# Kernel optimization log

Hardware: AMD Instinct MI355X
Metric: run time of the kernel (lower is better)

Reference implementation:

```python
import jax, jax.numpy as jnp
import numpy as np

ALPHA = 0.2  # LeakyReLU negative slope
NEG_INF = -9e15

def setup_inputs() -> dict:
    key = jax.random.key(0)
    k1, k2, k3, k4 = jax.random.split(key, 4)
    N, F_in, F_out = 8192, 256, 64
    h = jax.random.normal(k1, (N, F_in), dtype=jnp.float32)
    adj = jax.random.randint(k2, (N, N), 0, 2, dtype=jnp.int32)
    # xavier_uniform with gain=1.414
    def xavier(k, shape, gain=1.414):
        fan_in, fan_out = shape[0], shape[1]
        limit = gain * np.sqrt(6.0 / (fan_in + fan_out))
        return jax.random.uniform(k, shape, jnp.float32, -limit, limit)
    W = xavier(k3, (F_in, F_out))
    a = xavier(k4, (2 * F_out, 1))
    return {"h": h, "adj": adj, "W": W, "a": a}

def reference(h, adj, W, a):
    # Wh: (N, F_out)
    Wh = h @ W
    F_out = Wh.shape[1]
    a1 = a[:F_out, 0]   # (F_out,)
    a2 = a[F_out:, 0]   # (F_out,)
    # e_ij = LeakyReLU(Wh_i . a1 + Wh_j . a2)  -- equivalent to a^T [Wh_i || Wh_j]
    e = jax.nn.leaky_relu((Wh @ a1)[:, None] + (Wh @ a2)[None, :], negative_slope=ALPHA)
    scores = jnp.where(adj > 0, e, NEG_INF)
    attention = jax.nn.softmax(scores, axis=1)  # (N, N)
    h_prime = attention @ Wh                    # (N, F_out)
    return jax.nn.elu(h_prime)  # concat=True path
```

## Files before the change

### kernel.cpp

```cpp
#include <hip/hip_runtime.h>
#include <hip/hip_bf16.h>

#define N 8192
#define FIN 256
#define FOUT 64
#define NSLICE 8
#define SLICE_J (N / NSLICE)
#define NEG_INF -9.0e15f

typedef __attribute__((ext_vector_type(8))) short short8;
typedef __attribute__((ext_vector_type(4))) float f32x4;

static __device__ __forceinline__ short f2bf(float v) {
    __hip_bfloat16 b = __float2bfloat16(v);
    return __builtin_bit_cast(short, b);
}
static __device__ __forceinline__ float bf2f(short s) {
    unsigned u = ((unsigned)(unsigned short)s) << 16;
    return __builtin_bit_cast(float, u);
}

__global__ __launch_bounds__(256) void k_wh(const float* __restrict__ h,
                                            const float* __restrict__ W,
                                            const float* __restrict__ a,
                                            float* __restrict__ Wh,
                                            float* __restrict__ s1,
                                            float* __restrict__ s2) {
    int wave = threadIdx.x >> 6, lane = threadIdx.x & 63;
    int i = blockIdx.x * 4 + wave;
    const float* hrow = h + (size_t)i * FIN;
    float acc = 0.f;
#pragma unroll 8
    for (int k = 0; k < FIN; k += 4) {
        float4 hv = *(const float4*)(hrow + k);
        acc += hv.x * W[(k + 0) * FOUT + lane];
        acc += hv.y * W[(k + 1) * FOUT + lane];
        acc += hv.z * W[(k + 2) * FOUT + lane];
        acc += hv.w * W[(k + 3) * FOUT + lane];
    }
    Wh[(size_t)i * FOUT + lane] = acc;
    float v1 = acc * a[lane];
    float v2 = acc * a[FOUT + lane];
#pragma unroll
    for (int off = 32; off; off >>= 1) {
        v1 += __shfl_xor(v1, off);
        v2 += __shfl_xor(v2, off);
    }
    if (lane == 0) { s1[i] = v1; s2[i] = v2; }
}

__global__ __launch_bounds__(256) void k_repack(const float* __restrict__ Wh,
                                                short* __restrict__ WhB) {
    int t = blockIdx.x * 256 + threadIdx.x;
    int lane = t & 63, ft = (t >> 6) & 3, jt = t >> 8;
    int g = lane >> 4, r = lane & 15;
    short8 w;
#pragma unroll
    for (int q = 0; q < 8; ++q) {
        float v = Wh[(size_t)(jt * 32 + g * 8 + q) * FOUT + ft * 16 + r];
        w[q] = f2bf(v);
    }
    *((short8*)WhB + t) = w;
}

__global__ __launch_bounds__(128) void k_flash(const int* __restrict__ adj,
                                               const short* __restrict__ WhB,
                                               const float* __restrict__ s1,
                                               const float* __restrict__ s2,
                                               float* __restrict__ pO,
                                               float* __restrict__ pm,
                                               float* __restrict__ pl) {
    int rb = blockIdx.x / NSLICE, sl = blockIdx.x % NSLICE;
    int wave = threadIdx.x >> 6, lane = threadIdx.x & 63;
    int r = lane & 15, g = lane >> 4;
    int row = rb * 32 + wave * 16 + r;

    __shared__ __align__(16) float s2s[SLICE_J];
    for (int t = threadIdx.x; t < SLICE_J; t += 128) s2s[t] = s2[sl * SLICE_J + t];
    __syncthreads();

    float s1i = s1[row];
    float m = NEG_INF, l = 0.f;
    f32x4 acc0 = {0.f, 0.f, 0.f, 0.f};
    f32x4 acc1 = {0.f, 0.f, 0.f, 0.f};
    f32x4 acc2 = {0.f, 0.f, 0.f, 0.f};
    f32x4 acc3 = {0.f, 0.f, 0.f, 0.f};

    const int* arow = adj + (size_t)row * N + sl * SLICE_J + g * 8;

    for (int step = 0; step < SLICE_J / 32; ++step) {
        int4 av0 = *(const int4*)(arow + step * 32);
        int4 av1 = *(const int4*)(arow + step * 32 + 4);
        float4 sv0 = *(const float4*)&s2s[step * 32 + g * 8];
        float4 sv1 = *(const float4*)&s2s[step * 32 + g * 8 + 4];

        auto ec = [&](int aval, float s2v) -> float {
            float x = s1i + s2v;
            x = x > 0.f ? x : 0.2f * x;
            return aval > 0 ? x : NEG_INF;
        };
        float e0 = ec(av0.x, sv0.x), e1 = ec(av0.y, sv0.y);
        float e2 = ec(av0.z, sv0.z), e3 = ec(av0.w, sv0.w);
        float e4 = ec(av1.x, sv1.x), e5 = ec(av1.y, sv1.y);
        float e6 = ec(av1.z, sv1.z), e7 = ec(av1.w, sv1.w);

        float cmax = fmaxf(fmaxf(fmaxf(e0, e1), fmaxf(e2, e3)),
                           fmaxf(fmaxf(e4, e5), fmaxf(e6, e7)));
        cmax = fmaxf(cmax, __shfl_xor(cmax, 16));
        cmax = fmaxf(cmax, __shfl_xor(cmax, 32));
        float mnew = fmaxf(m, cmax);
        float scale = __expf(m - mnew);

        short8 af;
        float csum = 0.f;
        {
            float p0 = __expf(e0 - mnew), p1 = __expf(e1 - mnew);
            float p2 = __expf(e2 - mnew), p3 = __expf(e3 - mnew);
            float p4 = __expf(e4 - mnew), p5 = __expf(e5 - mnew);
            float p6 = __expf(e6 - mnew), p7 = __expf(e7 - mnew);
            af[0] = f2bf(p0); af[1] = f2bf(p1); af[2] = f2bf(p2); af[3] = f2bf(p3);
            af[4] = f2bf(p4); af[5] = f2bf(p5); af[6] = f2bf(p6); af[7] = f2bf(p7);
            csum = bf2f(af[0]) + bf2f(af[1]) + bf2f(af[2]) + bf2f(af[3]) +
                   bf2f(af[4]) + bf2f(af[5]) + bf2f(af[6]) + bf2f(af[7]);
        }
        csum += __shfl_xor(csum, 16);
        csum += __shfl_xor(csum, 32);
        l = l * scale + csum;
        m = mnew;

        float sc0 = __shfl(scale, g * 4 + 0);
        float sc1 = __shfl(scale, g * 4 + 1);
        float sc2 = __shfl(scale, g * 4 + 2);
        float sc3 = __shfl(scale, g * 4 + 3);
        acc0[0] *= sc0; acc0[1] *= sc1; acc0[2] *= sc2; acc0[3] *= sc3;
        acc1[0] *= sc0; acc1[1] *= sc1; acc1[2] *= sc2; acc1[3] *= sc3;
        acc2[0] *= sc0; acc2[1] *= sc1; acc2[2] *= sc2; acc2[3] *= sc3;
        acc3[0] *= sc0; acc3[1] *= sc1; acc3[2] *= sc2; acc3[3] *= sc3;

        int jt = sl * (SLICE_J / 32) + step;
        const short8* bp = (const short8*)WhB + (size_t)jt * 256 + lane;
        acc0 = __builtin_amdgcn_mfma_f32_16x16x32_bf16(af, bp[0], acc0, 0, 0, 0);
        acc1 = __builtin_amdgcn_mfma_f32_16x16x32_bf16(af, bp[64], acc1, 0, 0, 0);
        acc2 = __builtin_amdgcn_mfma_f32_16x16x32_bf16(af, bp[128], acc2, 0, 0, 0);
        acc3 = __builtin_amdgcn_mfma_f32_16x16x32_bf16(af, bp[192], acc3, 0, 0, 0);
    }

    int base_row = rb * 32 + wave * 16;
    f32x4 accs[4] = {acc0, acc1, acc2, acc3};
#pragma unroll
    for (int nt = 0; nt < 4; ++nt) {
#pragma unroll
        for (int reg = 0; reg < 4; ++reg) {
            int orow = base_row + g * 4 + reg;
            pO[((size_t)orow * NSLICE + sl) * FOUT + nt * 16 + r] = accs[nt][reg];
        }
    }
    if (lane < 16) {
        pm[(size_t)row * NSLICE + sl] = m;
        pl[(size_t)row * NSLICE + sl] = l;
    }
}

__global__ __launch_bounds__(256) void k_merge(const float* __restrict__ pO,
                                               const float* __restrict__ pm,
                                               const float* __restrict__ pl,
                                               float* __restrict__ out) {
    int t = blockIdx.x * 256 + threadIdx.x;
    int row = t >> 6, f = t & 63;
    float ms[NSLICE];
    float M = NEG_INF;
#pragma unroll
    for (int s = 0; s < NSLICE; ++s) {
        ms[s] = pm[(size_t)row * NSLICE + s];
        M = fmaxf(M, ms[s]);
    }
    float L = 0.f, O = 0.f;
#pragma unroll
    for (int s = 0; s < NSLICE; ++s) {
        float w = __expf(ms[s] - M);
        L += pl[(size_t)row * NSLICE + s] * w;
        O += pO[((size_t)row * NSLICE + s) * FOUT + f] * w;
    }
    float x = O / L;
    out[t] = x > 0.f ? x : expm1f(x);
}

extern "C" void kernel_launch(void* const* d_in, const int* in_sizes, int n_in,
                              void* d_out, int out_size, void* d_ws, size_t ws_size,
                              hipStream_t stream) {
    const float* h   = (const float*)d_in[0];
    const int*   adj = (const int*)d_in[1];
    const float* W   = (const float*)d_in[2];
    const float* a   = (const float*)d_in[3];
    float* out = (float*)d_out;

    char* ws = (char*)d_ws;
    float* Wh  = (float*)ws;
    short* WhB = (short*)(ws + (2u << 20));
    float* s1  = (float*)(ws + (3u << 20));
    float* s2  = (float*)(ws + (3u << 20) + 32768);
    float* pO  = (float*)(ws + (4u << 20));
    float* pm  = (float*)(ws + (20u << 20));
    float* pl  = (float*)(ws + (20u << 20) + (256u << 10));

    k_wh<<<N / 4, 256, 0, stream>>>(h, W, a, Wh, s1, s2);
    k_repack<<<(N / 32) * 4 * 64 / 256, 256, 0, stream>>>(Wh, WhB);
    k_flash<<<(N / 32) * NSLICE, 128, 0, stream>>>(adj, WhB, s1, s2, pO, pm, pl);
    k_merge<<<N * FOUT / 256, 256, 0, stream>>>(pO, pm, pl, out);
}
```

Measured before the change: 122.2 us.

## Replace online softmax with precomputed global row max bound

```diff
diff --git a/kernel.cpp b/kernel.cpp
--- a/kernel.cpp
+++ b/kernel.cpp
@@ -7,6 +7,7 @@
 #define NSLICE 8
 #define SLICE_J (N / NSLICE)
 #define NEG_INF -9.0e15f
+#define L2E 1.4426950408889634f
 
 typedef __attribute__((ext_vector_type(8))) short short8;
 typedef __attribute__((ext_vector_type(4))) float f32x4;
@@ -18,6 +19,9 @@
 static __device__ __forceinline__ float bf2f(short s) {
     unsigned u = ((unsigned)(unsigned short)s) << 16;
     return __builtin_bit_cast(float, u);
+}
+static __device__ __forceinline__ float exp2fast(float x) {
+    return __builtin_amdgcn_exp2f(x);
 }
 
 __global__ __launch_bounds__(256) void k_wh(const float* __restrict__ h,
@@ -46,7 +50,23 @@
         v1 += __shfl_xor(v1, off);
         v2 += __shfl_xor(v2, off);
     }
-    if (lane == 0) { s1[i] = v1; s2[i] = v2; }
+    if (lane == 0) { s1[i] = v1 * L2E; s2[i] = v2 * L2E; }
+}
+
+__global__ __launch_bounds__(256) void k_max(const float* __restrict__ s2,
+                                             float* __restrict__ maxs2) {
+    int t = threadIdx.x;
+    float m = NEG_INF;
+    for (int i = t; i < N; i += 256) m = fmaxf(m, s2[i]);
+#pragma unroll
+    for (int off = 32; off; off >>= 1) m = fmaxf(m, __shfl_xor(m, off));
+    __shared__ float red[4];
+    if ((t & 63) == 0) red[t >> 6] = m;
+    __syncthreads();
+    if (t == 0) {
+        float r = fmaxf(fmaxf(red[0], red[1]), fmaxf(red[2], red[3]));
+        maxs2[0] = r;
+    }
 }
 
 __global__ __launch_bounds__(256) void k_repack(const float* __restrict__ Wh,
@@ -67,8 +87,8 @@
                                                const short* __restrict__ WhB,
                                                const float* __restrict__ s1,
                                                const float* __restrict__ s2,
+                                               const float* __restrict__ maxs2,
                                                float* __restrict__ pO,
-                                               float* __restrict__ pm,
                                                float* __restrict__ pl) {
     int rb = blockIdx.x / NSLICE, sl = blockIdx.x % NSLICE;
     int wave = threadIdx.x >> 6, lane = threadIdx.x & 63;
@@ -80,7 +100,10 @@
     __syncthreads();
 
     float s1i = s1[row];
-    float m = NEG_INF, l = 0.f;
+    float xm = s1i + maxs2[0];
+    float Mp = fmaxf(xm, 0.2f * xm);
+
+    float l = 0.f;
     f32x4 acc0 = {0.f, 0.f, 0.f, 0.f};
     f32x4 acc1 = {0.f, 0.f, 0.f, 0.f};
     f32x4 acc2 = {0.f, 0.f, 0.f, 0.f};
@@ -88,54 +111,28 @@
 
     const int* arow = adj + (size_t)row * N + sl * SLICE_J + g * 8;
 
+#pragma unroll 2
     for (int step = 0; step < SLICE_J / 32; ++step) {
         int4 av0 = *(const int4*)(arow + step * 32);
         int4 av1 = *(const int4*)(arow + step * 32 + 4);
         float4 sv0 = *(const float4*)&s2s[step * 32 + g * 8];
         float4 sv1 = *(const float4*)&s2s[step * 32 + g * 8 + 4];
 
-        auto ec = [&](int aval, float s2v) -> float {
+        short8 af;
+        auto pc = [&](int aval, float s2v) -> short {
             float x = s1i + s2v;
-            x = x > 0.f ? x : 0.2f * x;
-            return aval > 0 ? x : NEG_INF;
+            float lr = fmaxf(x, 0.2f * x);
+            float p = exp2fast(lr - Mp);
+            p = aval > 0 ? p : 0.f;
+            return f2bf(p);
         };
-        float e0 = ec(av0.x, sv0.x), e1 = ec(av0.y, sv0.y);
-        float e2 = ec(av0.z, sv0.z), e3 = ec(av0.w, sv0.w);
-        float e4 = ec(av1.x, sv1.x), e5 = ec(av1.y, sv1.y);
-        float e6 = ec(av1.z, sv1.z), e7 = ec(av1.w, sv1.w);
+        af[0] = pc(av0.x, sv0.x); af[1] = pc(av0.y, sv0.y);
+        af[2] = pc(av0.z, sv0.z); af[3] = pc(av0.w, sv0.w);
+        af[4] = pc(av1.x, sv1.x); af[5] = pc(av1.y, sv1.y);
+        af[6] = pc(av1.z, sv1.z); af[7] = pc(av1.w, sv1.w);
 
-        float cmax = fmaxf(fmaxf(fmaxf(e0, e1), fmaxf(e2, e3)),
-                           fmaxf(fmaxf(e4, e5), fmaxf(e6, e7)));
-        cmax = fmaxf(cmax, __shfl_xor(cmax, 16));
-        cmax = fmaxf(cmax, __shfl_xor(cmax, 32));
-        float mnew = fmaxf(m, cmax);
-        float scale = __expf(m - mnew);
-
-        short8 af;
-        float csum = 0.f;
-        {
-            float p0 = __expf(e0 - mnew), p1 = __expf(e1 - mnew);
-            float p2 = __expf(e2 - mnew), p3 = __expf(e3 - mnew);
-            float p4 = __expf(e4 - mnew), p5 = __expf(e5 - mnew);
-            float p6 = __expf(e6 - mnew), p7 = __expf(e7 - mnew);
-            af[0] = f2bf(p0); af[1] = f2bf(p1); af[2] = f2bf(p2); af[3] = f2bf(p3);
-            af[4] = f2bf(p4); af[5] = f2bf(p5); af[6] = f2bf(p6); af[7] = f2bf(p7);
-            csum = bf2f(af[0]) + bf2f(af[1]) + bf2f(af[2]) + bf2f(af[3]) +
-                   bf2f(af[4]) + bf2f(af[5]) + bf2f(af[6]) + bf2f(af[7]);
-        }
-        csum += __shfl_xor(csum, 16);
-        csum += __shfl_xor(csum, 32);
-        l = l * scale + csum;
-        m = mnew;
-
-        float sc0 = __shfl(scale, g * 4 + 0);
-        float sc1 = __shfl(scale, g * 4 + 1);
-        float sc2 = __shfl(scale, g * 4 + 2);
-        float sc3 = __shfl(scale, g * 4 + 3);
-        acc0[0] *= sc0; acc0[1] *= sc1; acc0[2] *= sc2; acc0[3] *= sc3;
-        acc1[0] *= sc0; acc1[1] *= sc1; acc1[2] *= sc2; acc1[3] *= sc3;
-        acc2[0] *= sc0; acc2[1] *= sc1; acc2[2] *= sc2; acc2[3] *= sc3;
-        acc3[0] *= sc0; acc3[1] *= sc1; acc3[2] *= sc2; acc3[3] *= sc3;
+        l += bf2f(af[0]) + bf2f(af[1]) + bf2f(af[2]) + bf2f(af[3]) +
+             bf2f(af[4]) + bf2f(af[5]) + bf2f(af[6]) + bf2f(af[7]);
 
         int jt = sl * (SLICE_J / 32) + step;
         const short8* bp = (const short8*)WhB + (size_t)jt * 256 + lane;
@@ -144,6 +141,9 @@
         acc2 = __builtin_amdgcn_mfma_f32_16x16x32_bf16(af, bp[128], acc2, 0, 0, 0);
         acc3 = __builtin_amdgcn_mfma_f32_16x16x32_bf16(af, bp[192], acc3, 0, 0, 0);
     }
+
+    l += __shfl_xor(l, 16);
+    l += __shfl_xor(l, 32);
 
     int base_row = rb * 32 + wave * 16;
     f32x4 accs[4] = {acc0, acc1, acc2, acc3};
@@ -155,31 +155,19 @@
             pO[((size_t)orow * NSLICE + sl) * FOUT + nt * 16 + r] = accs[nt][reg];
         }
     }
-    if (lane < 16) {
-        pm[(size_t)row * NSLICE + sl] = m;
-        pl[(size_t)row * NSLICE + sl] = l;
-    }
+    if (lane < 16) pl[(size_t)row * NSLICE + sl] = l;
 }
 
 __global__ __launch_bounds__(256) void k_merge(const float* __restrict__ pO,
-                                               const float* __restrict__ pm,
                                                const float* __restrict__ pl,
                                                float* __restrict__ out) {
     int t = blockIdx.x * 256 + threadIdx.x;
     int row = t >> 6, f = t & 63;
-    float ms[NSLICE];
-    float M = NEG_INF;
-#pragma unroll
-    for (int s = 0; s < NSLICE; ++s) {
-        ms[s] = pm[(size_t)row * NSLICE + s];
-        M = fmaxf(M, ms[s]);
-    }
     float L = 0.f, O = 0.f;
 #pragma unroll
     for (int s = 0; s < NSLICE; ++s) {
-        float w = __expf(ms[s] - M);
-        L += pl[(size_t)row * NSLICE + s] * w;
-        O += pO[((size_t)row * NSLICE + s) * FOUT + f] * w;
+        L += pl[(size_t)row * NSLICE + s];
+        O += pO[((size_t)row * NSLICE + s) * FOUT + f];
     }
     float x = O / L;
     out[t] = x > 0.f ? x : expm1f(x);
@@ -195,16 +183,17 @@
     float* out = (float*)d_out;
 
     char* ws = (char*)d_ws;
-    float* Wh  = (float*)ws;
-    short* WhB = (short*)(ws + (2u << 20));
-    float* s1  = (float*)(ws + (3u << 20));
-    float* s2  = (float*)(ws + (3u << 20) + 32768);
-    float* pO  = (float*)(ws + (4u << 20));
-    float* pm  = (float*)(ws + (20u << 20));
-    float* pl  = (float*)(ws + (20u << 20) + (256u << 10));
+    float* Wh    = (float*)ws;
+    short* WhB   = (short*)(ws + (2u << 20));
+    float* s1    = (float*)(ws + (3u << 20));
+    float* s2    = (float*)(ws + (3u << 20) + 32768);
+    float* maxs2 = (float*)(ws + (3u << 20) + 65536);
+    float* pO    = (float*)(ws + (4u << 20));
+    float* pl    = (float*)(ws + (20u << 20));
 
     k_wh<<<N / 4, 256, 0, stream>>>(h, W, a, Wh, s1, s2);
+    k_max<<<1, 256, 0, stream>>>(s2, maxs2);
     k_repack<<<(N / 32) * 4 * 64 / 256, 256, 0, stream>>>(Wh, WhB);
-    k_flash<<<(N / 32) * NSLICE, 128, 0, stream>>>(adj, WhB, s1, s2, pO, pm, pl);
-    k_merge<<<N * FOUT / 256, 256, 0, stream>>>(pO, pm, pl, out);
+    k_flash<<<(N / 32) * NSLICE, 128, 0, stream>>>(adj, WhB, s1, s2, maxs2, pO, pl);
+    k_merge<<<N * FOUT / 256, 256, 0, stream>>>(pO, pl, out);
 }
```

Measured after the change: 122.0 us. About the same (-0.2%).
